# Kernel tuning notes

Hardware: AMD Instinct MI355X
Metric: run time of the kernel (lower is better)

The kernel has to match this reference:

```python
import jax, jax.numpy as jnp
import numpy as np

T, B, IN, H, F, OUT = 2048, 32, 256, 512, 2048, 256


def setup_inputs() -> dict:
    key = jax.random.key(0)
    ks = jax.random.split(key, 9)
    s_in = 1.0 / np.sqrt(IN)
    s_h = 1.0 / np.sqrt(H)
    s_f = 1.0 / np.sqrt(F)
    return {
        "x": jax.random.normal(ks[0], (T, B, IN), dtype=jnp.float32),
        "Wg": jax.random.uniform(ks[1], (H, IN), jnp.float32, -s_in, s_in),
        "bg": jax.random.uniform(ks[2], (H,), jnp.float32, -s_in, s_in),
        "Wi": jax.random.uniform(ks[3], (H, IN), jnp.float32, -s_in, s_in),
        "bi": jax.random.uniform(ks[4], (H,), jnp.float32, -s_in, s_in),
        "W1": jax.random.uniform(ks[5], (F, H), jnp.float32, -s_h, s_h),
        "b1": jax.random.uniform(ks[6], (F,), jnp.float32, -s_h, s_h),
        "W2": jax.random.uniform(ks[7], (OUT, F), jnp.float32, -s_f, s_f),
        "b2": jax.random.uniform(ks[8], (OUT,), jnp.float32, -s_f, s_f),
    }


def _gilr_scan(a, b):
    # h_t = a_t * h_{t-1} + b_t with h_0 = 0  ->  parallel associative scan over time
    def combine(c1, c2):
        a1, b1 = c1
        a2, b2 = c2
        return (a1 * a2, b1 * a2 + b2)
    _, h = jax.lax.associative_scan(combine, (a, b), axis=0)
    return h


def reference(x, Wg, bg, Wi, bi, W1, b1, W2, b2):
    # x: (T, B, IN)
    g = jax.nn.sigmoid(jnp.einsum("tbi,hi->tbh", x, Wg) + bg)  # (T,B,H)
    i = jnp.tanh(jnp.einsum("tbi,hi->tbh", x, Wi) + bi)        # (T,B,H)
    h = _gilr_scan(g, (1.0 - g) * i)                             # (T,B,H)
    z = jax.nn.gelu(jnp.einsum("tbh,fh->tbf", h, W1) + b1, approximate=False)
    out = jnp.einsum("tbf,of->tbo", z, W2) + b2                  # (T,B,OUT)
    return out
```

## Files before the change

### kernel.cpp

```cpp
#include <hip/hip_runtime.h>
#include <hip/hip_fp16.h>
#include <math.h>


#define IN_DIM 256
#define H_DIM 512
#define F_DIM 2048
#define OUT_DIM 256

typedef _Float16 f16;
typedef _Float16 f16x8 __attribute__((ext_vector_type(8)));
typedef float f32x4 __attribute__((ext_vector_type(4)));

#define AS3(p) ((__attribute__((address_space(3))) void*)(p))
#define AS1(p) ((const __attribute__((address_space(1))) void*)(p))
#define MFMA16(d, x, y) d = __builtin_amdgcn_mfma_f32_16x16x32_f16(x, y, d, 0, 0, 0)


__global__ void cvt_kernel(const float* __restrict__ in, f16* __restrict__ out, int n8) {
  int i = blockIdx.x * blockDim.x + threadIdx.x;
  if (i >= n8) return;
  const float4* p = (const float4*)in + (size_t)i * 2;
  float4 a = p[0], b = p[1];
  f16x8 o = { (f16)a.x, (f16)a.y, (f16)a.z, (f16)a.w,
              (f16)b.x, (f16)b.y, (f16)b.z, (f16)b.w };
  *((f16x8*)out + i) = o;
}

__global__ void bias_cat_kernel(const float* __restrict__ bg, const float* __restrict__ bi,
                                float* __restrict__ bgi) {
  int t = threadIdx.x;
  bgi[t] = (t < 512) ? bg[t] : bi[t - 512];
}

__device__ __forceinline__ float sigmoid_fast(float v) {
  return __builtin_amdgcn_rcpf(1.0f + __expf(-v));
}
__device__ __forceinline__ float tanh_fast(float v) {
  return 1.0f - 2.0f * __builtin_amdgcn_rcpf(__expf(2.0f * v) + 1.0f);
}
__device__ __forceinline__ float gelu_fast(float v) {
  float u = v * v;
  float y = v * fmaf(0.0713548353f, u, 1.59576912161f);
  return v * __builtin_amdgcn_rcpf(1.0f + __expf(-y));
}


__global__ __launch_bounds__(256, 2) void gemm1_k(
    const f16* __restrict__ A, const f16* __restrict__ Bw,
    const float* __restrict__ bias, f16* __restrict__ Cout) {
  constexpr int LDA = 256, LDB = 256, LDC = 1024, NT = 8;
  __shared__ f16 lds[24576];
  const int tid = threadIdx.x, wid = tid >> 6, lane = tid & 63;
  const int lr = lane & 15;
  const int bid = blockIdx.x;
  const int m0 = ((bid & 7) * 32 + (bid >> 6)) * 256;
  const int n0 = ((bid >> 3) & 7) * 128;
  const int wr = (wid >> 1) * 128, wc = (wid & 1) * 64;

  const f16* srcA[4];
  const f16* srcB[2];
#pragma unroll
  for (int q = 0; q < 4; ++q) {
    int s = wid * 256 + q * 64 + lane;
    int row = s >> 2, g = (s & 3) ^ ((row >> 1) & 3);
    srcA[q] = A + (size_t)(m0 + row) * LDA + g * 8;
  }
#pragma unroll
  for (int q = 0; q < 2; ++q) {
    int s = wid * 128 + q * 64 + lane;
    int row = s >> 2, g = (s & 3) ^ ((row >> 1) & 3);
    srcB[q] = Bw + (size_t)(n0 + row) * LDB + g * 8;
  }
  auto stage = [&](int buf, int kt) {
#pragma unroll
    for (int q = 0; q < 4; ++q)
      __builtin_amdgcn_global_load_lds(AS1(srcA[q] + kt * 32),
          AS3(lds + buf * 8192 + wid * 2048 + q * 512), 16, 0, 0);
#pragma unroll
    for (int q = 0; q < 2; ++q)
      __builtin_amdgcn_global_load_lds(AS1(srcB[q] + kt * 32),
          AS3(lds + 16384 + buf * 4096 + wid * 1024 + q * 512), 16, 0, 0);
  };

  const int qsf = (((lane >> 4) ^ ((lr >> 1) & 3)) << 3);
  f32x4 acc[8][4] = {};
  stage(0, 0);
  for (int kt = 0; kt < NT; ++kt) {
    const int cur = kt & 1;
    __syncthreads();
    if (kt + 1 < NT) stage(cur ^ 1, kt + 1);
    f16x8 af[8], bf[4];
#pragma unroll
    for (int mi = 0; mi < 8; ++mi)
      af[mi] = *(const f16x8*)(lds + cur * 8192 + (wr + mi * 16 + lr) * 32 + qsf);
#pragma unroll
    for (int ni = 0; ni < 4; ++ni)
      bf[ni] = *(const f16x8*)(lds + 16384 + cur * 4096 + (wc + ni * 16 + lr) * 32 + qsf);
#pragma unroll
    for (int mi = 0; mi < 8; ++mi)
#pragma unroll
      for (int ni = 0; ni < 4; ++ni)
        MFMA16(acc[mi][ni], af[mi], bf[ni]);
  }

  __syncthreads();
  const bool sig = n0 < 512;
  f16* ep = lds + wid * 4096;
  const int rq = (lane >> 4) * 4;
#pragma unroll
  for (int h = 0; h < 2; ++h) {
#pragma unroll
    for (int mi = 0; mi < 4; ++mi) {
#pragma unroll
      for (int ni = 0; ni < 4; ++ni) {
        float bv = bias[n0 + wc + ni * 16 + lr];
        int cc = ni * 2 + (lr >> 3);
#pragma unroll
        for (int j = 0; j < 4; ++j) {
          int lrow = mi * 16 + rq + j;
          float v = acc[h * 4 + mi][ni][j] + bv;
          float av = sig ? sigmoid_fast(v) : tanh_fast(v);
          ep[lrow * 64 + ((cc ^ (lrow & 7)) << 3) + (lr & 7)] = (f16)av;
        }
      }
    }
    asm volatile("s_waitcnt lgkmcnt(0)" ::: "memory");
    __builtin_amdgcn_sched_barrier(0);
#pragma unroll
    for (int t = 0; t < 8; ++t) {
      int idx = t * 64 + lane;
      int row = idx >> 3, c = idx & 7;
      f16x8 v = *(const f16x8*)(ep + row * 64 + ((c ^ (row & 7)) << 3));
      *(f16x8*)(Cout + (size_t)(m0 + wr + h * 64 + row) * LDC + n0 + wc + c * 8) = v;
    }
    asm volatile("s_waitcnt lgkmcnt(0)" ::: "memory");
    __builtin_amdgcn_sched_barrier(0);
  }
}


__global__ __launch_bounds__(256, 2) void gemm2_k(
    const f16* __restrict__ A, const f16* __restrict__ Bw,
    const float* __restrict__ bias, f16* __restrict__ Cout) {
  constexpr int LDA = 1024, LDB = 512, LDC = 2048, NT = 16;
  __shared__ f16 lds[24576];
  const int tid = threadIdx.x, wid = tid >> 6, lane = tid & 63;
  const int lr = lane & 15;
  const int bid = blockIdx.x;
  const int m0 = ((bid & 7) * 8 + (bid >> 7)) * 256;
  const int n0 = ((bid >> 3) & 15) * 128;
  const int wr = (wid >> 1) * 128, wc = (wid & 1) * 64;

  const f16* srcA[4];
  const f16* srcB[2];
#pragma unroll
  for (int q = 0; q < 4; ++q) {
    int s = wid * 256 + q * 64 + lane;
    int row = s >> 2, g = (s & 3) ^ ((row >> 1) & 3);
    srcA[q] = A + (size_t)(m0 + row) * LDA + g * 8;
  }
#pragma unroll
  for (int q = 0; q < 2; ++q) {
    int s = wid * 128 + q * 64 + lane;
    int row = s >> 2, g = (s & 3) ^ ((row >> 1) & 3);
    srcB[q] = Bw + (size_t)(n0 + row) * LDB + g * 8;
  }
  auto stage = [&](int buf, int kt) {
#pragma unroll
    for (int q = 0; q < 4; ++q)
      __builtin_amdgcn_global_load_lds(AS1(srcA[q] + kt * 32),
          AS3(lds + buf * 8192 + wid * 2048 + q * 512), 16, 0, 0);
#pragma unroll
    for (int q = 0; q < 2; ++q)
      __builtin_amdgcn_global_load_lds(AS1(srcB[q] + kt * 32),
          AS3(lds + 16384 + buf * 4096 + wid * 1024 + q * 512), 16, 0, 0);
  };

  const int qsf = (((lane >> 4) ^ ((lr >> 1) & 3)) << 3);
  f32x4 acc[8][4] = {};
  stage(0, 0);
  for (int kt = 0; kt < NT; ++kt) {
    const int cur = kt & 1;
    __syncthreads();
    if (kt + 1 < NT) stage(cur ^ 1, kt + 1);
    f16x8 af[8], bf[4];
#pragma unroll
    for (int mi = 0; mi < 8; ++mi)
      af[mi] = *(const f16x8*)(lds + cur * 8192 + (wr + mi * 16 + lr) * 32 + qsf);
#pragma unroll
    for (int ni = 0; ni < 4; ++ni)
      bf[ni] = *(const f16x8*)(lds + 16384 + cur * 4096 + (wc + ni * 16 + lr) * 32 + qsf);
#pragma unroll
    for (int mi = 0; mi < 8; ++mi)
#pragma unroll
      for (int ni = 0; ni < 4; ++ni)
        MFMA16(acc[mi][ni], af[mi], bf[ni]);
  }

  __syncthreads();
  f16* ep = lds + wid * 4096;
  const int rq = (lane >> 4) * 4;
#pragma unroll
  for (int h = 0; h < 2; ++h) {
#pragma unroll
    for (int mi = 0; mi < 4; ++mi) {
#pragma unroll
      for (int ni = 0; ni < 4; ++ni) {
        float bv = bias[n0 + wc + ni * 16 + lr];
        int cc = ni * 2 + (lr >> 3);
#pragma unroll
        for (int j = 0; j < 4; ++j) {
          int lrow = mi * 16 + rq + j;
          float v = gelu_fast(acc[h * 4 + mi][ni][j] + bv);
          ep[lrow * 64 + ((cc ^ (lrow & 7)) << 3) + (lr & 7)] = (f16)v;
        }
      }
    }
    asm volatile("s_waitcnt lgkmcnt(0)" ::: "memory");
    __builtin_amdgcn_sched_barrier(0);
#pragma unroll
    for (int t = 0; t < 8; ++t) {
      int idx = t * 64 + lane;
      int row = idx >> 3, c = idx & 7;
      f16x8 v = *(const f16x8*)(ep + row * 64 + ((c ^ (row & 7)) << 3));
      *(f16x8*)(Cout + (size_t)(m0 + wr + h * 64 + row) * LDC + n0 + wc + c * 8) = v;
    }
    asm volatile("s_waitcnt lgkmcnt(0)" ::: "memory");
    __builtin_amdgcn_sched_barrier(0);
  }
}


__global__ __launch_bounds__(256, 2) void gemm2_kb(
    const f16* __restrict__ A, const f16* __restrict__ Bw,
    const float* __restrict__ bias, f16* __restrict__ Cout) {
  constexpr int LDA = 1024, LDB = 512, LDC = 2048, NT = 8;
  __shared__ f16 lds[24576];
  const int tid = threadIdx.x, wid = tid >> 6, lane = tid & 63;
  const int lr = lane & 15;
  const int bid = blockIdx.x;
  const int m0 = ((bid & 7) * 8 + (bid >> 7)) * 256;
  const int n0 = ((bid >> 3) & 15) * 128;
  const int wr = (wid >> 1) * 128, wc = (wid & 1) * 64;

  const f16* srcA[8];
  const f16* srcB[4];
#pragma unroll
  for (int q = 0; q < 8; ++q) {
    int s = wid * 512 + q * 64 + lane;
    int row = s >> 3, g = (s & 7) ^ (row & 7);
    srcA[q] = A + (size_t)(m0 + row) * LDA + g * 8;
  }
#pragma unroll
  for (int q = 0; q < 4; ++q) {
    int s = wid * 256 + q * 64 + lane;
    int row = s >> 3, g = (s & 7) ^ (row & 7);
    srcB[q] = Bw + (size_t)(n0 + row) * LDB + g * 8;
  }
  auto stage = [&](int kt) {
#pragma unroll
    for (int q = 0; q < 8; ++q)
      __builtin_amdgcn_global_load_lds(AS1(srcA[q] + kt * 64),
          AS3(lds + wid * 4096 + q * 512), 16, 0, 0);
#pragma unroll
    for (int q = 0; q < 4; ++q)
      __builtin_amdgcn_global_load_lds(AS1(srcB[q] + kt * 64),
          AS3(lds + 16384 + wid * 2048 + q * 512), 16, 0, 0);
  };

  const int qs0 = (((lane >> 4) ^ (lr & 7)) << 3);
  const int qs1 = (((4 + (lane >> 4)) ^ (lr & 7)) << 3);
  f32x4 acc[8][4] = {};
  for (int kt = 0; kt < NT; ++kt) {
    stage(kt);
    __syncthreads();
#pragma unroll
    for (int kk = 0; kk < 2; ++kk) {
      const int qs = kk ? qs1 : qs0;
      f16x8 af[8], bf[4];
#pragma unroll
      for (int mi = 0; mi < 8; ++mi)
        af[mi] = *(const f16x8*)(lds + (wr + mi * 16 + lr) * 64 + qs);
#pragma unroll
      for (int ni = 0; ni < 4; ++ni)
        bf[ni] = *(const f16x8*)(lds + 16384 + (wc + ni * 16 + lr) * 64 + qs);
#pragma unroll
      for (int mi = 0; mi < 8; ++mi)
#pragma unroll
        for (int ni = 0; ni < 4; ++ni)
          MFMA16(acc[mi][ni], af[mi], bf[ni]);
    }
    __syncthreads();
  }

  f16* ep = lds + wid * 4096;
  const int rq = (lane >> 4) * 4;
#pragma unroll
  for (int h = 0; h < 2; ++h) {
#pragma unroll
    for (int mi = 0; mi < 4; ++mi) {
#pragma unroll
      for (int ni = 0; ni < 4; ++ni) {
        float bv = bias[n0 + wc + ni * 16 + lr];
        int cc = ni * 2 + (lr >> 3);
#pragma unroll
        for (int j = 0; j < 4; ++j) {
          int lrow = mi * 16 + rq + j;
          float v = gelu_fast(acc[h * 4 + mi][ni][j] + bv);
          ep[lrow * 64 + ((cc ^ (lrow & 7)) << 3) + (lr & 7)] = (f16)v;
        }
      }
    }
    asm volatile("s_waitcnt lgkmcnt(0)" ::: "memory");
    __builtin_amdgcn_sched_barrier(0);
#pragma unroll
    for (int t = 0; t < 8; ++t) {
      int idx = t * 64 + lane;
      int row = idx >> 3, c = idx & 7;
      f16x8 v = *(const f16x8*)(ep + row * 64 + ((c ^ (row & 7)) << 3));
      *(f16x8*)(Cout + (size_t)(m0 + wr + h * 64 + row) * LDC + n0 + wc + c * 8) = v;
    }
    asm volatile("s_waitcnt lgkmcnt(0)" ::: "memory");
    __builtin_amdgcn_sched_barrier(0);
  }
}


__global__ __launch_bounds__(256, 2) void gemm3_k(
    const f16* __restrict__ A, const f16* __restrict__ Bw,
    const float* __restrict__ bias, float* __restrict__ Cout) {
  constexpr int LDA = 2048, LDB = 2048, LDC = 256, NT = 32;
  __shared__ f16 lds[2][2][128][64];
  const int tid = threadIdx.x, wid = tid >> 6, lane = tid & 63;
  const int bid = blockIdx.x;
  const int m0 = ((bid & 7) * 16 + (bid >> 4)) * 128;
  const int n0 = ((bid >> 3) & 1) * 128;
  const int wr = (wid >> 1) * 64, wc = (wid & 1) * 64;

  auto stage = [&](int buf, int kt) {
    const f16* ga = A + (size_t)m0 * LDA + kt * 64;
    const f16* gb = Bw + (size_t)n0 * LDB + kt * 64;
    f16* la = &lds[buf][0][0][0];
    f16* lb = &lds[buf][1][0][0];
#pragma unroll
    for (int q = 0; q < 4; ++q) {
      int seg = (wid << 2) + q;
      int s = seg * 64 + lane;
      int row = s >> 3, col = (s & 7) << 3;
      __builtin_amdgcn_global_load_lds(AS1(ga + (size_t)row * LDA + col),
                                       AS3(la + seg * 512), 16, 0, 0);
      __builtin_amdgcn_global_load_lds(AS1(gb + (size_t)row * LDB + col),
                                       AS3(lb + seg * 512), 16, 0, 0);
    }
  };

  f32x4 acc[4][4] = {};
  stage(0, 0);
  for (int kt = 0; kt < NT; ++kt) {
    __syncthreads();
    if (kt + 1 < NT) stage((kt + 1) & 1, kt + 1);
    f16(*At)[64] = lds[kt & 1][0];
    f16(*Bt)[64] = lds[kt & 1][1];
    const int r = lane & 15, cg = (lane >> 4) << 3;
#pragma unroll
    for (int kk = 0; kk < 2; ++kk) {
      f16x8 af[4], bf[4];
#pragma unroll
      for (int i = 0; i < 4; ++i)
        af[i] = *(const f16x8*)&At[wr + i * 16 + r][kk * 32 + cg];
#pragma unroll
      for (int i = 0; i < 4; ++i)
        bf[i] = *(const f16x8*)&Bt[wc + i * 16 + r][kk * 32 + cg];
#pragma unroll
      for (int mi = 0; mi < 4; ++mi)
#pragma unroll
        for (int ni = 0; ni < 4; ++ni)
          MFMA16(acc[mi][ni], af[mi], bf[ni]);
    }
  }
  const int r = lane & 15, rq = (lane >> 4) * 4;
#pragma unroll
  for (int ni = 0; ni < 4; ++ni) {
    int col = n0 + wc + ni * 16 + r;
    float bv = bias[col];
#pragma unroll
    for (int mi = 0; mi < 4; ++mi) {
#pragma unroll
      for (int j = 0; j < 4; ++j) {
        int row = m0 + wr + mi * 16 + rq + j;
        Cout[(size_t)row * LDC + col] = acc[mi][ni][j] + bv;
      }
    }
  }
}


#define NCH 16384
#define NCHUNK 32
#define CLEN 64

__global__ void scan_p1(const f16* __restrict__ ab, float* __restrict__ cA,
                        float* __restrict__ cH) {
  int ch = blockIdx.x * 256 + threadIdx.x;
  int c = blockIdx.y;
  const f16* pg = ab + (size_t)(c * CLEN) * 32768 + (ch >> 9) * 1024 + (ch & 511);
  const f16* pi = pg + 512;
  float A = 1.f, Hl = 0.f;
  for (int t = 0; t < CLEN; ++t) {
    float g = (float)pg[0];
    float ii = (float)pi[0];
    Hl = fmaf(g, Hl - ii, ii);
    A *= g;
    pg += 32768; pi += 32768;
  }
  cA[c * NCH + ch] = A;
  cH[c * NCH + ch] = Hl;
}

__global__ void scan_p2(const float* __restrict__ cA, const float* __restrict__ cH,
                        float* __restrict__ st) {
  int ch = blockIdx.x * 256 + threadIdx.x;
  float h0 = 0.f;
  for (int c = 0; c < NCHUNK; ++c) {
    st[c * NCH + ch] = h0;
    h0 = cA[c * NCH + ch] * h0 + cH[c * NCH + ch];
  }
}

__global__ void scan_p3(f16* __restrict__ ab, const float* __restrict__ st) {
  int ch = blockIdx.x * 256 + threadIdx.x;
  int c = blockIdx.y;
  f16* pg = ab + (size_t)(c * CLEN) * 32768 + (ch >> 9) * 1024 + (ch & 511);
  const f16* pi = pg + 512;
  float hv = st[c * NCH + ch];
  for (int t = 0; t < CLEN; ++t) {
    float g = (float)pg[0];
    float ii = (float)pi[0];
    hv = fmaf(g, hv - ii, ii);
    pg[0] = (f16)hv;
    pg += 32768; pi += 32768;
  }
}


extern "C" void kernel_launch(void* const* d_in, const int* in_sizes, int n_in,
                              void* d_out, int out_size, void* d_ws, size_t ws_size,
                              hipStream_t stream) {
  const float* x  = (const float*)d_in[0];
  const float* Wg = (const float*)d_in[1];
  const float* bg = (const float*)d_in[2];
  const float* Wi = (const float*)d_in[3];
  const float* bi = (const float*)d_in[4];
  const float* W1 = (const float*)d_in[5];
  const float* b1 = (const float*)d_in[6];
  const float* W2 = (const float*)d_in[7];
  const float* b2 = (const float*)d_in[8];
  float* out = (float*)d_out;

  char* ws = (char*)d_ws;
  f16*   wgi16 = (f16*)(ws + 0);
  f16*   w116  = (f16*)(ws + 524288);
  f16*   w216  = (f16*)(ws + 2621440);
  float* bgi   = (float*)(ws + 3670016);
  f16*   x16   = (f16*)(ws + 4194304);
  f16*   ab16  = (f16*)(ws + 37748736);
  float* cA    = (float*)(ws + 171966464);
  float* cH    = (float*)(ws + 174063616);
  float* st    = (float*)(ws + 176160768);
  f16*   z16   = (f16*)(ws + 178257920);
  if (ws_size < 245366784) return;

  cvt_kernel<<<64, 256, 0, stream>>>(Wg, wgi16, 16384);
  cvt_kernel<<<64, 256, 0, stream>>>(Wi, wgi16 + 131072, 16384);
  cvt_kernel<<<512, 256, 0, stream>>>(W1, w116, 131072);
  cvt_kernel<<<256, 256, 0, stream>>>(W2, w216, 65536);
  bias_cat_kernel<<<1, 1024, 0, stream>>>(bg, bi, bgi);
  cvt_kernel<<<8192, 256, 0, stream>>>(x, x16, 2097152);

  gemm1_k<<<2048, 256, 0, stream>>>(x16, wgi16, bgi, ab16);

  scan_p1<<<dim3(64, NCHUNK), 256, 0, stream>>>(ab16, cA, cH);
  scan_p2<<<64, 256, 0, stream>>>(cA, cH, st);
  scan_p3<<<dim3(64, NCHUNK), 256, 0, stream>>>(ab16, st);

  for (int s = 0; s < 4; ++s) {
    const f16* hs = ab16 + (size_t)s * 16384 * 1024;
    if (s < 2)
      gemm2_k<<<1024, 256, 0, stream>>>(hs, w116, b1, z16);
    else
      gemm2_kb<<<1024, 256, 0, stream>>>(hs, w116, b1, z16);
    gemm3_k<<<256, 256, 0, stream>>>(z16, w216, b2, out + (size_t)s * 16384 * 256);
  }
}
```

Before: 497.7 us.

## Fuse weight casts, split gemm1 into two tile variants, add triple-buffered gemm2

The four weight-conversion launches are merged into one cvt_w kernel. gemm1 is replaced by two variants with 128x128 tiles run on the two halves of the rows: a double-buffered one with higher occupancy and a triple-buffered one with explicit vmcnt waits. The gemm2 path for the last two slices becomes a 512-thread, 256x256-tile kernel with a three-stage LDS pipeline. These aim to cut launch overhead and improve load/compute overlap and occupancy, at the cost of more LDS per block and more fragile hand-written wait counts.

```diff
diff --git a/kernel.cpp b/kernel.cpp
--- a/kernel.cpp
+++ b/kernel.cpp
@@ -27,6 +27,21 @@
   *((f16x8*)out + i) = o;
 }
 
+__global__ void cvt_w(const float* __restrict__ Wg, const float* __restrict__ Wi,
+                      const float* __restrict__ W1, const float* __restrict__ W2,
+                      f16* __restrict__ wgi, f16* __restrict__ w1, f16* __restrict__ w2) {
+  int i = blockIdx.x * 256 + threadIdx.x;
+  const float* src; f16* dst; int l;
+  if (i < 16384)       { l = i;          src = Wg + (size_t)l * 8; dst = wgi + (size_t)l * 8; }
+  else if (i < 32768)  { l = i - 16384;  src = Wi + (size_t)l * 8; dst = wgi + 131072 + (size_t)l * 8; }
+  else if (i < 163840) { l = i - 32768;  src = W1 + (size_t)l * 8; dst = w1 + (size_t)l * 8; }
+  else                 { l = i - 163840; src = W2 + (size_t)l * 8; dst = w2 + (size_t)l * 8; }
+  float4 a = ((const float4*)src)[0], b = ((const float4*)src)[1];
+  f16x8 o = { (f16)a.x, (f16)a.y, (f16)a.z, (f16)a.w,
+              (f16)b.x, (f16)b.y, (f16)b.z, (f16)b.w };
+  *(f16x8*)dst = o;
+}
+
 __global__ void bias_cat_kernel(const float* __restrict__ bg, const float* __restrict__ bi,
                                 float* __restrict__ bgi) {
   int t = threadIdx.x;
@@ -46,59 +61,51 @@
 }
 
 
-__global__ __launch_bounds__(256, 2) void gemm1_k(
+__global__ __launch_bounds__(256, 4) void gemm1_t2(
     const f16* __restrict__ A, const f16* __restrict__ Bw,
     const float* __restrict__ bias, f16* __restrict__ Cout) {
   constexpr int LDA = 256, LDB = 256, LDC = 1024, NT = 8;
-  __shared__ f16 lds[24576];
+  __shared__ f16 lds[2][2][128][32];
   const int tid = threadIdx.x, wid = tid >> 6, lane = tid & 63;
-  const int lr = lane & 15;
   const int bid = blockIdx.x;
-  const int m0 = ((bid & 7) * 32 + (bid >> 6)) * 256;
+  const int m0 = ((bid & 7) * 32 + (bid >> 6)) * 128;
   const int n0 = ((bid >> 3) & 7) * 128;
-  const int wr = (wid >> 1) * 128, wc = (wid & 1) * 64;
-
-  const f16* srcA[4];
-  const f16* srcB[2];
-#pragma unroll
-  for (int q = 0; q < 4; ++q) {
-    int s = wid * 256 + q * 64 + lane;
+  const int wr = (wid >> 1) * 64, wc = (wid & 1) * 64;
+
+  const f16* srcA[2]; const f16* srcB[2];
+#pragma unroll
+  for (int q = 0; q < 2; ++q) {
+    int s = (wid * 2 + q) * 64 + lane;
     int row = s >> 2, g = (s & 3) ^ ((row >> 1) & 3);
     srcA[q] = A + (size_t)(m0 + row) * LDA + g * 8;
-  }
-#pragma unroll
-  for (int q = 0; q < 2; ++q) {
-    int s = wid * 128 + q * 64 + lane;
-    int row = s >> 2, g = (s & 3) ^ ((row >> 1) & 3);
     srcB[q] = Bw + (size_t)(n0 + row) * LDB + g * 8;
   }
   auto stage = [&](int buf, int kt) {
-#pragma unroll
-    for (int q = 0; q < 4; ++q)
-      __builtin_amdgcn_global_load_lds(AS1(srcA[q] + kt * 32),
-          AS3(lds + buf * 8192 + wid * 2048 + q * 512), 16, 0, 0);
-#pragma unroll
-    for (int q = 0; q < 2; ++q)
-      __builtin_amdgcn_global_load_lds(AS1(srcB[q] + kt * 32),
-          AS3(lds + 16384 + buf * 4096 + wid * 1024 + q * 512), 16, 0, 0);
+    f16* la = &lds[buf][0][0][0] + (wid * 2) * 512;
+    f16* lb = &lds[buf][1][0][0] + (wid * 2) * 512;
+#pragma unroll
+    for (int q = 0; q < 2; ++q) {
+      __builtin_amdgcn_global_load_lds(AS1(srcA[q] + kt * 32), AS3(la + q * 512), 16, 0, 0);
+      __builtin_amdgcn_global_load_lds(AS1(srcB[q] + kt * 32), AS3(lb + q * 512), 16, 0, 0);
+    }
   };
-
-  const int qsf = (((lane >> 4) ^ ((lr >> 1) & 3)) << 3);
-  f32x4 acc[8][4] = {};
+  const int r = lane & 15;
+  const int cs = (((lane >> 4) ^ ((lane >> 1) & 3)) << 3);
+
+  f32x4 acc[4][4] = {};
   stage(0, 0);
   for (int kt = 0; kt < NT; ++kt) {
-    const int cur = kt & 1;
     __syncthreads();
-    if (kt + 1 < NT) stage(cur ^ 1, kt + 1);
-    f16x8 af[8], bf[4];
-#pragma unroll
-    for (int mi = 0; mi < 8; ++mi)
-      af[mi] = *(const f16x8*)(lds + cur * 8192 + (wr + mi * 16 + lr) * 32 + qsf);
-#pragma unroll
-    for (int ni = 0; ni < 4; ++ni)
-      bf[ni] = *(const f16x8*)(lds + 16384 + cur * 4096 + (wc + ni * 16 + lr) * 32 + qsf);
-#pragma unroll
-    for (int mi = 0; mi < 8; ++mi)
+    if (kt + 1 < NT) stage((kt + 1) & 1, kt + 1);
+    f16(*At)[32] = lds[kt & 1][0];
+    f16(*Bt)[32] = lds[kt & 1][1];
+    f16x8 af[4], bf[4];
+#pragma unroll
+    for (int i = 0; i < 4; ++i) af[i] = *(const f16x8*)&At[wr + i * 16 + r][cs];
+#pragma unroll
+    for (int i = 0; i < 4; ++i) bf[i] = *(const f16x8*)&Bt[wc + i * 16 + r][cs];
+#pragma unroll
+    for (int mi = 0; mi < 4; ++mi)
 #pragma unroll
       for (int ni = 0; ni < 4; ++ni)
         MFMA16(acc[mi][ni], af[mi], bf[ni]);
@@ -106,36 +113,119 @@
 
   __syncthreads();
   const bool sig = n0 < 512;
-  f16* ep = lds + wid * 4096;
+  f16* ep = &lds[0][0][0][0] + wid * 4096;
   const int rq = (lane >> 4) * 4;
 #pragma unroll
-  for (int h = 0; h < 2; ++h) {
+  for (int ni = 0; ni < 4; ++ni) {
+    float bv = bias[n0 + wc + ni * 16 + r];
+    int cc = ni * 2 + (r >> 3);
 #pragma unroll
     for (int mi = 0; mi < 4; ++mi) {
 #pragma unroll
-      for (int ni = 0; ni < 4; ++ni) {
-        float bv = bias[n0 + wc + ni * 16 + lr];
-        int cc = ni * 2 + (lr >> 3);
-#pragma unroll
-        for (int j = 0; j < 4; ++j) {
-          int lrow = mi * 16 + rq + j;
-          float v = acc[h * 4 + mi][ni][j] + bv;
-          float av = sig ? sigmoid_fast(v) : tanh_fast(v);
-          ep[lrow * 64 + ((cc ^ (lrow & 7)) << 3) + (lr & 7)] = (f16)av;
-        }
+      for (int j = 0; j < 4; ++j) {
+        int lrow = mi * 16 + rq + j;
+        float v = acc[mi][ni][j] + bv;
+        float av = sig ? sigmoid_fast(v) : tanh_fast(v);
+        ep[lrow * 64 + ((cc ^ (lrow & 7)) << 3) + (r & 7)] = (f16)av;
       }
     }
-    asm volatile("s_waitcnt lgkmcnt(0)" ::: "memory");
-    __builtin_amdgcn_sched_barrier(0);
-#pragma unroll
-    for (int t = 0; t < 8; ++t) {
-      int idx = t * 64 + lane;
-      int row = idx >> 3, c = idx & 7;
-      f16x8 v = *(const f16x8*)(ep + row * 64 + ((c ^ (row & 7)) << 3));
-      *(f16x8*)(Cout + (size_t)(m0 + wr + h * 64 + row) * LDC + n0 + wc + c * 8) = v;
-    }
-    asm volatile("s_waitcnt lgkmcnt(0)" ::: "memory");
-    __builtin_amdgcn_sched_barrier(0);
+  }
+  asm volatile("s_waitcnt lgkmcnt(0)" ::: "memory");
+  __builtin_amdgcn_sched_barrier(0);
+#pragma unroll
+  for (int t = 0; t < 8; ++t) {
+    int idx = t * 64 + lane;
+    int row = idx >> 3, c = idx & 7;
+    f16x8 v = *(const f16x8*)(ep + row * 64 + ((c ^ (row & 7)) << 3));
+    *(f16x8*)(Cout + (size_t)(m0 + wr + row) * LDC + n0 + wc + c * 8) = v;
+  }
+}
+
+
+__global__ __launch_bounds__(256, 3) void gemm1_t3(
+    const f16* __restrict__ A, const f16* __restrict__ Bw,
+    const float* __restrict__ bias, f16* __restrict__ Cout) {
+  constexpr int LDA = 256, LDB = 256, LDC = 1024, NT = 8;
+  __shared__ f16 lds[3][2][128][32];
+  const int tid = threadIdx.x, wid = tid >> 6, lane = tid & 63;
+  const int bid = blockIdx.x;
+  const int m0 = ((bid & 7) * 32 + (bid >> 6)) * 128;
+  const int n0 = ((bid >> 3) & 7) * 128;
+  const int wr = (wid >> 1) * 64, wc = (wid & 1) * 64;
+
+  const f16* srcA[2]; const f16* srcB[2];
+#pragma unroll
+  for (int q = 0; q < 2; ++q) {
+    int s = (wid * 2 + q) * 64 + lane;
+    int row = s >> 2, g = (s & 3) ^ ((row >> 1) & 3);
+    srcA[q] = A + (size_t)(m0 + row) * LDA + g * 8;
+    srcB[q] = Bw + (size_t)(n0 + row) * LDB + g * 8;
+  }
+  auto stage = [&](int buf, int kt) {
+    f16* la = &lds[buf][0][0][0] + (wid * 2) * 512;
+    f16* lb = &lds[buf][1][0][0] + (wid * 2) * 512;
+#pragma unroll
+    for (int q = 0; q < 2; ++q) {
+      __builtin_amdgcn_global_load_lds(AS1(srcA[q] + kt * 32), AS3(la + q * 512), 16, 0, 0);
+      __builtin_amdgcn_global_load_lds(AS1(srcB[q] + kt * 32), AS3(lb + q * 512), 16, 0, 0);
+    }
+  };
+  const int r = lane & 15;
+  const int cs = (((lane >> 4) ^ ((lane >> 1) & 3)) << 3);
+
+  f32x4 acc[4][4] = {};
+  stage(0, 0); stage(1, 1);
+  asm volatile("s_waitcnt vmcnt(4)" ::: "memory");
+  __syncthreads();
+#pragma unroll
+  for (int kt = 0; kt < NT; ++kt) {
+    if (kt + 2 < NT) stage((kt + 2) % 3, kt + 2);
+    f16(*At)[32] = lds[kt % 3][0];
+    f16(*Bt)[32] = lds[kt % 3][1];
+    f16x8 af[4], bf[4];
+#pragma unroll
+    for (int i = 0; i < 4; ++i) af[i] = *(const f16x8*)&At[wr + i * 16 + r][cs];
+#pragma unroll
+    for (int i = 0; i < 4; ++i) bf[i] = *(const f16x8*)&Bt[wc + i * 16 + r][cs];
+#pragma unroll
+    for (int mi = 0; mi < 4; ++mi)
+#pragma unroll
+      for (int ni = 0; ni < 4; ++ni)
+        MFMA16(acc[mi][ni], af[mi], bf[ni]);
+    if (kt + 1 < NT) {
+      if (kt + 2 < NT) asm volatile("s_waitcnt vmcnt(4)" ::: "memory");
+      else             asm volatile("s_waitcnt vmcnt(0)" ::: "memory");
+      __syncthreads();
+    }
+  }
+
+  __syncthreads();
+  const bool sig = n0 < 512;
+  f16* ep = &lds[0][0][0][0] + wid * 4096;
+  const int rq = (lane >> 4) * 4;
+#pragma unroll
+  for (int ni = 0; ni < 4; ++ni) {
+    float bv = bias[n0 + wc + ni * 16 + r];
+    int cc = ni * 2 + (r >> 3);
+#pragma unroll
+    for (int mi = 0; mi < 4; ++mi) {
+#pragma unroll
+      for (int j = 0; j < 4; ++j) {
+        int lrow = mi * 16 + rq + j;
+        float v = acc[mi][ni][j] + bv;
+        float av = sig ? sigmoid_fast(v) : tanh_fast(v);
+        ep[lrow * 64 + ((cc ^ (lrow & 7)) << 3) + (r & 7)] = (f16)av;
+      }
+    }
+  }
+  asm volatile("s_waitcnt lgkmcnt(0)" ::: "memory");
+  __builtin_amdgcn_sched_barrier(0);
+#pragma unroll
+  for (int t = 0; t < 8; ++t) {
+    int idx = t * 64 + lane;
+    int row = idx >> 3, c = idx & 7;
+    f16x8 v = *(const f16x8*)(ep + row * 64 + ((c ^ (row & 7)) << 3));
+    *(f16x8*)(Cout + (size_t)(m0 + wr + row) * LDC + n0 + wc + c * 8) = v;
   }
 }
 
@@ -232,69 +322,67 @@
 }
 
 
-__global__ __launch_bounds__(256, 2) void gemm2_kb(
+__global__ __launch_bounds__(512, 2) void gemm2_q(
     const f16* __restrict__ A, const f16* __restrict__ Bw,
     const float* __restrict__ bias, f16* __restrict__ Cout) {
-  constexpr int LDA = 1024, LDB = 512, LDC = 2048, NT = 8;
-  __shared__ f16 lds[24576];
+  constexpr int LDA = 1024, LDB = 512, LDC = 2048, NT = 16;
+  __shared__ f16 lds[3][2][8192];
   const int tid = threadIdx.x, wid = tid >> 6, lane = tid & 63;
   const int lr = lane & 15;
   const int bid = blockIdx.x;
-  const int m0 = ((bid & 7) * 8 + (bid >> 7)) * 256;
-  const int n0 = ((bid >> 3) & 15) * 128;
-  const int wr = (wid >> 1) * 128, wc = (wid & 1) * 64;
-
-  const f16* srcA[8];
-  const f16* srcB[4];
-#pragma unroll
-  for (int q = 0; q < 8; ++q) {
-    int s = wid * 512 + q * 64 + lane;
-    int row = s >> 3, g = (s & 7) ^ (row & 7);
+  const int m0 = ((bid & 7) * 8 + (bid >> 6)) * 256;
+  const int n0 = ((bid >> 3) & 7) * 256;
+  const int wr = (wid >> 2) * 128, wc = (wid & 3) * 64;
+
+  const f16* srcA[2]; const f16* srcB[2];
+#pragma unroll
+  for (int q = 0; q < 2; ++q) {
+    int s = q * 512 + tid;
+    int row = s >> 2, g = (s & 3) ^ ((row >> 1) & 3);
     srcA[q] = A + (size_t)(m0 + row) * LDA + g * 8;
-  }
-#pragma unroll
-  for (int q = 0; q < 4; ++q) {
-    int s = wid * 256 + q * 64 + lane;
-    int row = s >> 3, g = (s & 7) ^ (row & 7);
     srcB[q] = Bw + (size_t)(n0 + row) * LDB + g * 8;
   }
-  auto stage = [&](int kt) {
-#pragma unroll
-    for (int q = 0; q < 8; ++q)
-      __builtin_amdgcn_global_load_lds(AS1(srcA[q] + kt * 64),
-          AS3(lds + wid * 4096 + q * 512), 16, 0, 0);
-#pragma unroll
-    for (int q = 0; q < 4; ++q)
-      __builtin_amdgcn_global_load_lds(AS1(srcB[q] + kt * 64),
-          AS3(lds + 16384 + wid * 2048 + q * 512), 16, 0, 0);
+  auto stage = [&](int buf, int kt) {
+#pragma unroll
+    for (int q = 0; q < 2; ++q) {
+      __builtin_amdgcn_global_load_lds(AS1(srcA[q] + kt * 32),
+          AS3(&lds[buf][0][0] + q * 4096 + wid * 512), 16, 0, 0);
+      __builtin_amdgcn_global_load_lds(AS1(srcB[q] + kt * 32),
+          AS3(&lds[buf][1][0] + q * 4096 + wid * 512), 16, 0, 0);
+    }
   };
 
-  const int qs0 = (((lane >> 4) ^ (lr & 7)) << 3);
-  const int qs1 = (((4 + (lane >> 4)) ^ (lr & 7)) << 3);
+  const int qsf = (((lane >> 4) ^ ((lr >> 1) & 3)) << 3);
   f32x4 acc[8][4] = {};
+  stage(0, 0); stage(1, 1);
+  asm volatile("s_waitcnt vmcnt(4)" ::: "memory");
+  __syncthreads();
+#pragma unroll
   for (int kt = 0; kt < NT; ++kt) {
-    stage(kt);
-    __syncthreads();
-#pragma unroll
-    for (int kk = 0; kk < 2; ++kk) {
-      const int qs = kk ? qs1 : qs0;
-      f16x8 af[8], bf[4];
-#pragma unroll
-      for (int mi = 0; mi < 8; ++mi)
-        af[mi] = *(const f16x8*)(lds + (wr + mi * 16 + lr) * 64 + qs);
+    if (kt + 2 < NT) stage((kt + 2) % 3, kt + 2);
+    const f16* La = &lds[kt % 3][0][0];
+    const f16* Lb = &lds[kt % 3][1][0];
+    f16x8 af[8], bf[4];
+#pragma unroll
+    for (int mi = 0; mi < 8; ++mi)
+      af[mi] = *(const f16x8*)(La + (wr + mi * 16 + lr) * 32 + qsf);
+#pragma unroll
+    for (int ni = 0; ni < 4; ++ni)
+      bf[ni] = *(const f16x8*)(Lb + (wc + ni * 16 + lr) * 32 + qsf);
+#pragma unroll
+    for (int mi = 0; mi < 8; ++mi)
 #pragma unroll
       for (int ni = 0; ni < 4; ++ni)
-        bf[ni] = *(const f16x8*)(lds + 16384 + (wc + ni * 16 + lr) * 64 + qs);
-#pragma unroll
-      for (int mi = 0; mi < 8; ++mi)
-#pragma unroll
-        for (int ni = 0; ni < 4; ++ni)
-          MFMA16(acc[mi][ni], af[mi], bf[ni]);
-    }
-    __syncthreads();
-  }
-
-  f16* ep = lds + wid * 4096;
+        MFMA16(acc[mi][ni], af[mi], bf[ni]);
+    if (kt + 1 < NT) {
+      if (kt + 2 < NT) asm volatile("s_waitcnt vmcnt(4)" ::: "memory");
+      else             asm volatile("s_waitcnt vmcnt(0)" ::: "memory");
+      __syncthreads();
+    }
+  }
+
+  __syncthreads();
+  f16* ep = &lds[0][0][0] + wid * 4096;
   const int rq = (lane >> 4) * 4;
 #pragma unroll
   for (int h = 0; h < 2; ++h) {
@@ -471,14 +559,13 @@
   f16*   z16   = (f16*)(ws + 178257920);
   if (ws_size < 245366784) return;
 
-  cvt_kernel<<<64, 256, 0, stream>>>(Wg, wgi16, 16384);
-  cvt_kernel<<<64, 256, 0, stream>>>(Wi, wgi16 + 131072, 16384);
-  cvt_kernel<<<512, 256, 0, stream>>>(W1, w116, 131072);
-  cvt_kernel<<<256, 256, 0, stream>>>(W2, w216, 65536);
+  cvt_w<<<896, 256, 0, stream>>>(Wg, Wi, W1, W2, wgi16, w116, w216);
   bias_cat_kernel<<<1, 1024, 0, stream>>>(bg, bi, bgi);
   cvt_kernel<<<8192, 256, 0, stream>>>(x, x16, 2097152);
 
-  gemm1_k<<<2048, 256, 0, stream>>>(x16, wgi16, bgi, ab16);
+  gemm1_t2<<<2048, 256, 0, stream>>>(x16, wgi16, bgi, ab16);
+  gemm1_t3<<<2048, 256, 0, stream>>>(x16 + (size_t)32768 * 256, wgi16, bgi,
+                                     ab16 + (size_t)32768 * 1024);
 
   scan_p1<<<dim3(64, NCHUNK), 256, 0, stream>>>(ab16, cA, cH);
   scan_p2<<<64, 256, 0, stream>>>(cA, cH, st);
@@ -489,7 +576,7 @@
     if (s < 2)
       gemm2_k<<<1024, 256, 0, stream>>>(hs, w116, b1, z16);
     else
-      gemm2_kb<<<1024, 256, 0, stream>>>(hs, w116, b1, z16);
+      gemm2_q<<<512, 512, 0, stream>>>(hs, w116, b1, z16);
     gemm3_k<<<256, 256, 0, stream>>>(z16, w216, b2, out + (size_t)s * 16384 * 256);
   }
 }
```

Result: faster. 482.9 us (-3.0%).
